# Optimization experiments

Measured on AMD Instinct MI355X. Metric: run time of the kernel, lower is better.

The kernel has to match this reference:

```python
import jax, jax.numpy as jnp
import numpy as np

# --- stochastic-computing constants (match FSUMGUCell defaults) ---
BW_W = 8                      # FSULinearPC weight bitstream bitwidth
BW_M = 4                      # FSUMul bitwidth (shift-register depth)
DEPTH = 10                    # FSUAdd accumulator depth
ACC_MAX = 2.0 ** (DEPTH - 2)  # +256
ACC_MIN = -ACC_MAX
NW = 2 ** BW_W
NM = 2 ** BW_M
# deterministic pseudo-random comparison sequences (stand-in for UnarySim Sobol RNG)
_RNG_W = jnp.asarray(np.random.RandomState(0).permutation(NW), dtype=jnp.float32)
_RNG_WI = jnp.asarray(np.random.RandomState(1).permutation(NW), dtype=jnp.float32)
_RNG_M = jnp.asarray(np.random.RandomState(2).permutation(NM), dtype=jnp.float32)


def _fsu_add(acc, s, offset, scale):
    # FSUAdd (bipolar): accumulate (parallel count - offset), clamp, emit bit when acc >= scale
    acc = jnp.clip(acc + s - offset, ACC_MIN, ACC_MAX)
    out = (acc >= scale).astype(jnp.float32)
    return acc - out * scale, out


def _linear_pc(x_aug, w_src, t):
    # FSULinearPC (bipolar): weight bits generated by rate coding (source > rng[t]),
    # XNOR with input bits, summed into a parallel count. x_aug: [B, F+1] (bias col of 1s).
    wb_p = (w_src > _RNG_W[t % NW]).astype(jnp.float32)   # [O, F+1]
    wb_i = (w_src > _RNG_WI[t % NW]).astype(jnp.float32)
    return x_aug @ wb_p.T + (1.0 - x_aug) @ (1.0 - wb_i).T


def _fsu_mul(state, in0, in1):
    # FSUMul non-static bipolar: estimate P(in1) with a BW_M-bit shift register,
    # regenerate a bit via rng comparison; XNOR-style pos/inv paths gated by in0,
    # with conditionally-advanced rng indices (enable-signal semantics).
    sr, idx_p, idx_i = state
    sr = jnp.concatenate([sr[1:], in1[None]], axis=0)      # shift in newest bit
    cnt = sr.sum(0) * (NM / BW_M)                          # scale count to rng range
    bit_p = (cnt > _RNG_M[idx_p % NM]).astype(jnp.float32)
    bit_i = (cnt > _RNG_M[idx_i % NM]).astype(jnp.float32)
    out = in0 * bit_p + (1.0 - in0) * (1.0 - bit_i)        # disjoint paths -> OR == +
    idx_p = idx_p + in0.astype(jnp.int32)
    idx_i = idx_i + (1 - in0.astype(jnp.int32))
    return (sr, idx_p, idx_i), out


def _w_src(w, b):
    # SourceGen bipolar: binary value in [-1,1] -> integer source in [0, 2^BW_W]
    aug = jnp.concatenate([w, b[:, None]], axis=1)
    return jnp.round((jnp.clip(aug, -1.0, 1.0) + 1.0) * 0.5 * NW)


def _forward(x_bits, hx0, weight_ih, bias_ih, weight_hh, bias_hh):
    T, B, I = x_bits.shape
    H = hx0.shape[1]
    src_ih = _w_src(weight_ih, bias_ih)   # [2H, I+1]
    src_hh = _w_src(weight_hh, bias_hh)   # [2H, H+1]
    ones_col = jnp.ones((B, 1), jnp.float32)
    acc0 = jnp.zeros((B, H), jnp.float32)
    sr0 = jnp.tile((jnp.arange(BW_M) % 2).astype(jnp.float32)[:, None, None], (1, B, H))
    mul0 = (sr0, jnp.zeros((B, H), jnp.int32), jnp.zeros((B, H), jnp.int32))
    off_fg = (I + H + 2 - 1) / 2.0        # entry=I+H+2, scaled=False -> scale=1

    def step(carry, xt):
        h, a1, a2, a3, a4, a5, a6, m1, m2, m3, t = carry
        gate_i = _linear_pc(jnp.concatenate([xt, ones_col], 1), src_ih, t)  # [B, 2H]
        gate_h = _linear_pc(jnp.concatenate([h, ones_col], 1), src_hh, t)
        i_f, i_n = gate_i[:, :H], gate_i[:, H:]
        h_f, h_n = gate_h[:, :H], gate_h[:, H:]
        a1, fg_in = _fsu_add(a1, i_f + h_f, off_fg, 1.0)
        a2, fg = _fsu_add(a2, fg_in + 1.0, 0.0, 2.0)          # scaled (x+1)/2 hardsigmoid
        a3, h_n_bit = _fsu_add(a3, h_n, H / 2.0, 1.0)          # entry=H+1
        m1, ng_prod = _fsu_mul(m1, fg, h_n_bit)
        a4, i_n_bit = _fsu_add(a4, i_n, I / 2.0, 1.0)          # entry=I+1
        a5, ng = _fsu_add(a5, i_n_bit + ng_prod, 0.5, 1.0)     # entry=2
        m2, fgi_prod = _fsu_mul(m2, 1.0 - fg, ng)
        m3, fg_prod = _fsu_mul(m3, fg, h)
        a6, hy = _fsu_add(a6, ng + fgi_prod + fg_prod, 1.0, 1.0)  # entry=3
        return (hy, a1, a2, a3, a4, a5, a6, m1, m2, m3, t + 1), hy

    carry0 = (hx0, acc0, acc0, acc0, acc0, acc0, acc0, mul0, mul0, mul0, jnp.int32(0))
    _, hy_stream = jax.lax.scan(step, carry0, x_bits)
    return hy_stream  # [T, B, H] unary bitstream of hidden state


def setup_inputs():
    key = jax.random.key(0)
    ks = jax.random.split(key, 6)
    T, B, I, H = 64, 128, 1024, 1024
    x_bits = jax.random.bernoulli(ks[0], 0.5, (T, B, I)).astype(jnp.float32)
    hx0 = jax.random.bernoulli(ks[1], 0.5, (B, H)).astype(jnp.float32)
    weight_ih = jax.random.uniform(ks[2], (2 * H, I), jnp.float32, -1.0, 1.0)
    bias_ih = jax.random.uniform(ks[3], (2 * H,), jnp.float32, -1.0, 1.0)
    weight_hh = jax.random.uniform(ks[4], (2 * H, H), jnp.float32, -1.0, 1.0)
    bias_hh = jax.random.uniform(ks[5], (2 * H,), jnp.float32, -1.0, 1.0)
    return {"x_bits": x_bits, "hx0": hx0, "weight_ih": weight_ih, "bias_ih": bias_ih,
            "weight_hh": weight_hh, "bias_hh": bias_hh}


def reference(x_bits, hx0, weight_ih, bias_ih, weight_hh, bias_hh):
    return _forward(x_bits, hx0, weight_ih, bias_ih, weight_hh, bias_hh)
```

## Files before the change

### kernel.cpp

```cpp
#include <hip/hip_runtime.h>


#define NBLK 256
#define NTHR 512

#define WS_BAR_SUB   0u
#define WS_BAR_MST   1024u
#define WS_BAR_FLG   2048u
#define WS_RNGW   8192u
#define WS_RNGWI  9216u
#define WS_RNGM   10240u
#define WS_SRCB   12288u
#define WS_SRCW   20480u
#define WS_XP     8409088u
#define WS_HW     9457664u
#define WS_DT     9523200u
#define WS_MASKS  10571776u

struct SRng {
  unsigned mt[3][624];
  unsigned yb[3][624];
  unsigned draws[3][1248];
  int perm[3][256];
};
struct SC {
  unsigned short rows[16][1028];
  int rngw[64];
  int rngwi[64];
};
struct SL {
  unsigned long long mask2[64*34];
  unsigned xb[32*34];
  unsigned hb[32*34];
  unsigned hraw[64*17];
  int dl[64];
  int rngm[16];
};
union SU { SRng r; SC c; SL l; };

__device__ __forceinline__ unsigned mt_temper(unsigned y){
  y ^= y >> 11;
  y ^= (y << 7)  & 0x9d2c5680u;
  y ^= (y << 15) & 0xefc60000u;
  y ^= y >> 18;
  return y;
}

__device__ void mt_regen_serial(unsigned* mt){
  for (int i = 0; i < 624; i++){
    unsigned y = (mt[i] & 0x80000000u) | (mt[(i+1)%624] & 0x7fffffffu);
    mt[i] = mt[(i+397)%624] ^ (y >> 1) ^ ((y & 1u) ? 0x9908b0dfu : 0u);
  }
}

__device__ void rng_gen(SU* sm, int* rngw, int* rngwi, int* rngm){
  const int tid = threadIdx.x;
  const int wv = tid >> 6, lane = tid & 63;
  const bool act = (wv < 3);
  if (act && lane == 0){
    unsigned* mt = sm->r.mt[wv];
    mt[0] = (unsigned)wv;
    for (int i = 1; i < 624; i++)
      mt[i] = 1812433253u * (mt[i-1] ^ (mt[i-1] >> 30)) + (unsigned)i;
  }
  __syncthreads();
  for (int r = 0; r < 2; r++){
    if (act){
      unsigned* mt = sm->r.mt[wv]; unsigned* yb = sm->r.yb[wv];
      for (int i = lane; i < 623; i += 64)
        yb[i] = (mt[i] & 0x80000000u) | (mt[i+1] & 0x7fffffffu);
    }
    __syncthreads();
    if (act){
      unsigned* mt = sm->r.mt[wv]; unsigned* yb = sm->r.yb[wv];
      for (int i = lane; i < 227; i += 64){
        unsigned y = yb[i];
        mt[i] = mt[i+397] ^ (y >> 1) ^ ((y & 1u) ? 0x9908b0dfu : 0u);
      }
    }
    __syncthreads();
    if (act){
      unsigned* mt = sm->r.mt[wv]; unsigned* yb = sm->r.yb[wv];
      for (int i = 227 + lane; i < 454; i += 64){
        unsigned y = yb[i];
        mt[i] = mt[i-227] ^ (y >> 1) ^ ((y & 1u) ? 0x9908b0dfu : 0u);
      }
    }
    __syncthreads();
    if (act){
      unsigned* mt = sm->r.mt[wv]; unsigned* yb = sm->r.yb[wv];
      for (int i = 454 + lane; i < 624; i += 64){
        unsigned y = (i < 623) ? yb[i]
                   : ((mt[623] & 0x80000000u) | (mt[0] & 0x7fffffffu));
        mt[i] = mt[i-227] ^ (y >> 1) ^ ((y & 1u) ? 0x9908b0dfu : 0u);
      }
    }
    __syncthreads();
    if (act){
      unsigned* mt = sm->r.mt[wv];
      for (int i = lane; i < 624; i += 64)
        sm->r.draws[wv][r*624 + i] = mt_temper(mt[i]);
    }
    __syncthreads();
  }
  if (act && lane == 0){
    const int n = (wv == 2) ? 16 : 256;
    int* perm = sm->r.perm[wv];
    for (int i = 0; i < n; i++) perm[i] = i;
    int dp = 0, spos = 624;
    unsigned* mt = sm->r.mt[wv];
    for (int i = n - 1; i > 0; i--){
      unsigned mask = (unsigned)i;
      mask |= mask >> 1; mask |= mask >> 2; mask |= mask >> 4;
      mask |= mask >> 8; mask |= mask >> 16;
      unsigned v;
      do {
        unsigned d;
        if (dp < 1248) d = sm->r.draws[wv][dp++];
        else {
          if (spos >= 624){ mt_regen_serial(mt); spos = 0; }
          d = mt_temper(mt[spos++]);
        }
        v = d & mask;
      } while (v > (unsigned)i);
      int tmp = perm[i]; perm[i] = perm[v]; perm[v] = tmp;
    }
    int* dst = (wv == 0) ? rngw : (wv == 1) ? rngwi : rngm;
    for (int i = 0; i < n; i++) dst[i] = perm[i];
  }
}

__device__ __forceinline__ void gbar_full(unsigned char* ws, unsigned ep){
  __syncthreads();
  if (threadIdx.x == 0){
    __threadfence();
    unsigned* sub = (unsigned*)(ws + WS_BAR_SUB + (blockIdx.x & 7)*128);
    unsigned old = atomicAdd(sub, 1u);
    if (old == ep*32u - 1u){
      unsigned* mst = (unsigned*)(ws + WS_BAR_MST);
      unsigned mo = atomicAdd(mst, 1u);
      if (mo == ep*8u - 1u){
        for (int i = 0; i < 8; i++)
          __hip_atomic_store((unsigned*)(ws + WS_BAR_FLG + i*128), ep,
                             __ATOMIC_RELAXED, __HIP_MEMORY_SCOPE_AGENT);
      }
    }
    const unsigned* fl = (const unsigned*)(ws + WS_BAR_FLG + (blockIdx.x & 7)*128);
    while (__hip_atomic_load(fl, __ATOMIC_RELAXED, __HIP_MEMORY_SCOPE_AGENT) < ep)
      __builtin_amdgcn_s_sleep(8);
  }
  __syncthreads();
  __threadfence();
}

__device__ __forceinline__ int clampi(int v){
  v = v < -512 ? -512 : v;
  v = v >  512 ?  512 : v;
  return v;
}

__global__ void __launch_bounds__(NTHR)
fsu_kernel(const float* __restrict__ x, const float* __restrict__ hx0,
           const float* __restrict__ wih, const float* __restrict__ bih,
           const float* __restrict__ whh, const float* __restrict__ bhh,
           float* __restrict__ out, unsigned char* __restrict__ ws)
{
  __shared__ SU sm;
  const int tid = threadIdx.x;
  const int bid = blockIdx.x;

  int* rngw  = (int*)(ws + WS_RNGW);
  int* rngwi = (int*)(ws + WS_RNGWI);
  int* rngm  = (int*)(ws + WS_RNGM);
  unsigned short* srcb = (unsigned short*)(ws + WS_SRCB);
  unsigned short* srcw = (unsigned short*)(ws + WS_SRCW);
  unsigned* xp   = (unsigned*)(ws + WS_XP);
  unsigned long long* hw = (unsigned long long*)(ws + WS_HW);
  int* Dt = (int*)(ws + WS_DT);
  unsigned long long* masks = (unsigned long long*)(ws + WS_MASKS);

  if (bid == 0){
    rng_gen(&sm, rngw, rngwi, rngm);
  } else {
    const int gtid = (bid - 1)*NTHR + tid;
    const int lane = tid & 63;
    const int gw = gtid >> 6;
    const int nw = (NBLK-1)*(NTHR/64);
    const int nthr = (NBLK-1)*NTHR;
    for (int ch = gw; ch < 131072; ch += nw){
      float v = x[(size_t)ch*64 + lane];
      unsigned long long bal = __ballot(v != 0.0f);
      if ((lane & 31) == 0) xp[ch*2 + (lane >> 5)] = (unsigned)(bal >> lane);
    }
    for (int idx = gtid; idx < 4096; idx += nthr){
      int bg2 = idx >> 10, jt2 = (idx >> 4) & 63, rp2 = idx & 15;
      int r0 = bg2*32 + 2*rp2;
      unsigned v = 0;
      for (int j = 0; j < 16; j++){
        v |= (hx0[(size_t)r0*1024 + jt2*16 + j] != 0.0f) ? (1u<<j) : 0u;
        v |= (hx0[(size_t)(r0+1)*1024 + jt2*16 + j] != 0.0f) ? (1u<<(16+j)) : 0u;
      }
      hw[idx] = (unsigned long long)v;
    }
    for (int idx = gtid; idx < 4096*1024; idx += nthr){
      int c = idx >> 10, k = idx & 1023;
      float wv2 = (c < 2048) ? wih[(size_t)c*1024 + k] : whh[(size_t)(c - 2048)*1024 + k];
      float cl = fminf(fmaxf(wv2, -1.0f), 1.0f);
      srcw[idx] = (unsigned short)(int)rintf((cl + 1.0f)*0.5f*256.0f);
    }
    for (int c = gtid; c < 4096; c += nthr){
      float bv = (c < 2048) ? bih[c] : bhh[c - 2048];
      float cl = fminf(fmaxf(bv, -1.0f), 1.0f);
      srcb[c] = (unsigned short)(int)rintf((cl + 1.0f)*0.5f*256.0f);
    }
  }
  gbar_full(ws, 1u);

  {
    const int c0 = bid * 16;
    const unsigned* srcw32 = (const unsigned*)srcw;
    for (int q = tid; q < 16*512; q += NTHR){
      int r = q >> 9, w = q & 511;
      ((unsigned*)&sm.c.rows[r][0])[w] = srcw32[(size_t)(c0 + r)*512 + w];
    }
    if (tid < 64) sm.c.rngw[tid] = rngw[tid];
    if (tid >= 64 && tid < 128) sm.c.rngwi[tid - 64] = rngwi[tid - 64];
    __syncthreads();
    for (int rr = 0; rr < 2; rr++){
      int row = tid + rr*NTHR;
      int t = row >> 4, lc = row & 15, col = c0 + lc;
      int rp = sm.c.rngw[t], ri = sm.c.rngwi[t];
      int hi = rp > ri ? rp : ri;
      int lo1 = (rp < ri ? rp : ri) + 1;
      bool rihi = (ri >= rp);
      const unsigned* srow = (const unsigned*)&sm.c.rows[lc][0];
      unsigned long long* gdst = masks + ((size_t)t*4096 + col)*32;
      int cnti = 0;
      for (int w = 0; w < 32; w++){
        unsigned pos = 0, neg = 0;
        #pragma unroll
        for (int i2 = 15; i2 >= 0; i2--){
          unsigned v2 = srow[w*16 + i2];
          int vH = (int)(v2 >> 16);
          int vL = (int)(v2 & 0xFFFFu);
          pos = (pos << 1) | ((unsigned)(hi - vH) >> 31);
          neg = (neg << 1) | ((unsigned)(vH - lo1) >> 31);
          pos = (pos << 1) | ((unsigned)(hi - vL) >> 31);
          neg = (neg << 1) | ((unsigned)(vL - lo1) >> 31);
        }
        gdst[w] = (unsigned long long)pos | ((unsigned long long)neg << 32);
        cnti += rihi ? __popc(pos) : (32 - __popc(neg));
      }
      Dt[t*4096 + col] = 1024 - cnti + (((int)srcb[col] > rp) ? 1 : 0);
    }
  }
  gbar_full(ws, 2u);

  const int jt = bid & 63, bg = bid >> 6;
  const int j0 = jt * 16, b0 = bg * 32;
  const int b_l = tid >> 4, j_l = tid & 15;
  const int bglob = b0 + b_l;

  int hcur = (hx0[(size_t)bglob*1024 + j0 + j_l] != 0.0f) ? 1 : 0;
  int A1=0,A2=0,A3=0,A4=0,A5=0,A6=0;
  unsigned sr1=10u, sr2=10u, sr3=10u;
  int i1p=0,i1i=0,i2p=0,i2i=0,i3p=0,i3i=0;

  if (tid < 16) sm.l.rngm[tid] = rngm[tid];

  const unsigned* msrc = (const unsigned*)masks;
  unsigned* mlds = (unsigned*)sm.l.mask2;

  {
    #pragma unroll
    for (int i = 0; i < 8; i++){
      int q = tid + i*NTHR;
      int r = q >> 6, qq = q & 63;
      int c = (r >> 4)*1024 + j0 + (r & 15);
      mlds[r*68 + qq] = msrc[((size_t)0*4096 + c)*64 + qq];
    }
    #pragma unroll
    for (int i = 0; i < 2; i++){
      int q = tid + i*NTHR;
      int bb = q >> 5, w = q & 31;
      sm.l.xb[bb*34 + w] = xp[((size_t)0*128 + b0 + bb)*32 + w];
    }
    #pragma unroll
    for (int i = 0; i < 2; i++){
      int q = tid + i*NTHR;
      unsigned long long v = __hip_atomic_load(&hw[(size_t)bg*1024 + q],
                                               __ATOMIC_RELAXED,
                                               __HIP_MEMORY_SCOPE_AGENT);
      sm.l.hraw[(q >> 4)*17 + (q & 15)] = (unsigned)v;
    }
    if (tid < 64){
      int c = (tid >> 4)*1024 + j0 + (tid & 15);
      sm.l.dl[tid] = Dt[0*4096 + c];
    }
    __syncthreads();
    #pragma unroll
    for (int i = 0; i < 2; i++){
      int idx = tid + i*NTHR;
      int bb = idx >> 5, w = idx & 31;
      int rp = bb >> 1, sh = (bb & 1) << 4;
      unsigned lo = (sm.l.hraw[(2*w)*17 + rp] >> sh) & 0xFFFFu;
      unsigned hi = (sm.l.hraw[(2*w + 1)*17 + rp] >> sh) & 0xFFFFu;
      sm.l.hb[bb*34 + w] = lo | (hi << 16);
    }
    __syncthreads();
  }

  for (int t = 0; t < 64; t++){
    const int par = t & 1;

    int p0=0,n0=0,p1=0,n1=0,p2=0,n2=0,p3=0,n3=0;
    const ulonglong2* m0p = (const ulonglong2*)&sm.l.mask2[(0*16 + j_l)*34];
    const ulonglong2* m1p = (const ulonglong2*)&sm.l.mask2[(1*16 + j_l)*34];
    const ulonglong2* m2p = (const ulonglong2*)&sm.l.mask2[(2*16 + j_l)*34];
    const ulonglong2* m3p = (const ulonglong2*)&sm.l.mask2[(3*16 + j_l)*34];
    const uint2* xrow = (const uint2*)&sm.l.xb[b_l*34];
    const uint2* hrow = (const uint2*)&sm.l.hb[b_l*34];
    #pragma unroll
    for (int w2 = 0; w2 < 16; w2++){
      uint2 xv = xrow[w2], hv = hrow[w2];
      ulonglong2 a = m0p[w2];
      p0 += __popc(xv.x & (unsigned)a.x) + __popc(xv.y & (unsigned)a.y);
      n0 += __popc(xv.x & (unsigned)(a.x >> 32)) + __popc(xv.y & (unsigned)(a.y >> 32));
      ulonglong2 b = m1p[w2];
      p1 += __popc(xv.x & (unsigned)b.x) + __popc(xv.y & (unsigned)b.y);
      n1 += __popc(xv.x & (unsigned)(b.x >> 32)) + __popc(xv.y & (unsigned)(b.y >> 32));
      ulonglong2 c2 = m2p[w2];
      p2 += __popc(hv.x & (unsigned)c2.x) + __popc(hv.y & (unsigned)c2.y);
      n2 += __popc(hv.x & (unsigned)(c2.x >> 32)) + __popc(hv.y & (unsigned)(c2.y >> 32));
      ulonglong2 d = m3p[w2];
      p3 += __popc(hv.x & (unsigned)d.x) + __popc(hv.y & (unsigned)d.y);
      n3 += __popc(hv.x & (unsigned)(d.x >> 32)) + __popc(hv.y & (unsigned)(d.y >> 32));
    }
    const int g_if = sm.l.dl[0*16 + j_l] + p0 - n0;
    const int g_in = sm.l.dl[1*16 + j_l] + p1 - n1;
    const int g_hf = sm.l.dl[2*16 + j_l] + p2 - n2;
    const int g_hn = sm.l.dl[3*16 + j_l] + p3 - n3;

    int s1 = g_if + g_hf;
    A1 = clampi(A1 + 2*s1 - 2049);
    int fg_in = (A1 >= 2); A1 -= fg_in << 1;
    A2 = clampi(A2 + ((fg_in + 1) << 1));
    int fg = (A2 >= 4); A2 -= fg << 2;
    A3 = clampi(A3 + (g_hn << 1) - 1024);
    int hnb = (A3 >= 2); A3 -= hnb << 1;

    sr1 = ((sr1 >> 1) | ((unsigned)hnb << 3)) & 0xFu;
    int ng_prod;
    {
      int cv = __popc(sr1) << 2;
      int bp = cv > sm.l.rngm[i1p & 15];
      int bi = cv > sm.l.rngm[i1i & 15];
      ng_prod = fg ? bp : (1 - bi);
      i1p += fg; i1i += 1 - fg;
    }
    A4 = clampi(A4 + (g_in << 1) - 1024);
    int inb = (A4 >= 2); A4 -= inb << 1;
    A5 = clampi(A5 + ((inb + ng_prod) << 1) - 1);
    int ng = (A5 >= 2); A5 -= ng << 1;

    sr2 = ((sr2 >> 1) | ((unsigned)ng << 3)) & 0xFu;
    int fgi;
    {
      int cv = __popc(sr2) << 2;
      int bp = cv > sm.l.rngm[i2p & 15];
      int bi = cv > sm.l.rngm[i2i & 15];
      fgi = (1 - fg) ? bp : (1 - bi);
      i2p += 1 - fg; i2i += fg;
    }
    sr3 = ((sr3 >> 1) | ((unsigned)hcur << 3)) & 0xFu;
    int fgp;
    {
      int cv = __popc(sr3) << 2;
      int bp = cv > sm.l.rngm[i3p & 15];
      int bi = cv > sm.l.rngm[i3i & 15];
      fgp = fg ? bp : (1 - bi);
      i3p += fg; i3i += 1 - fg;
    }
    A6 = clampi(A6 + ((ng + fgi + fgp) << 1) - 2);
    int hy = (A6 >= 2); A6 -= hy << 1;
    hcur = hy;

    if (t < 63){
      unsigned long long bal = __ballot(hy);
      if ((tid & 31) == 0){
        unsigned data = (unsigned)(bal >> (tid & 32));
        unsigned long long val = (unsigned long long)data
                               | ((unsigned long long)(unsigned)(t + 1) << 32);
        __hip_atomic_store(
            &hw[(((size_t)(par ^ 1)*4 + bg)*64 + jt)*16 + (tid >> 5)], val,
            __ATOMIC_RELAXED, __HIP_MEMORY_SCOPE_AGENT);
      }
    }
    out[(size_t)t*131072 + (size_t)bglob*1024 + j0 + j_l] = (float)hy;

    if (t < 63){
      __syncthreads();

      unsigned mreg[8], xreg[2];
      int dreg = 0;
      #pragma unroll
      for (int i = 0; i < 8; i++){
        int q = tid + i*NTHR;
        int r = q >> 6, qq = q & 63;
        int c = (r >> 4)*1024 + j0 + (r & 15);
        mreg[i] = msrc[((size_t)(t+1)*4096 + c)*64 + qq];
      }
      #pragma unroll
      for (int i = 0; i < 2; i++){
        int q = tid + i*NTHR;
        int bb = q >> 5, w = q & 31;
        xreg[i] = xp[((size_t)(t+1)*128 + b0 + bb)*32 + w];
      }
      if (tid < 64){
        int c = (tid >> 4)*1024 + j0 + (tid & 15);
        dreg = Dt[(t+1)*4096 + c];
      }

      const unsigned ep = (unsigned)(t + 1);
      if (tid < 64){
        const unsigned long long* slot =
            &hw[(((size_t)(par ^ 1)*4 + bg)*64 + tid)*16];
        while (true){
          unsigned long long v = __hip_atomic_load(slot, __ATOMIC_RELAXED,
                                                   __HIP_MEMORY_SCOPE_AGENT);
          if (__all((int)((unsigned)(v >> 32) >= ep))) break;
          __builtin_amdgcn_s_sleep(2);
        }
      }
      __syncthreads();

      #pragma unroll
      for (int i = 0; i < 2; i++){
        int q = tid + i*NTHR;
        const unsigned long long* slot =
            &hw[((size_t)(par ^ 1)*4 + bg)*1024 + q];
        unsigned long long v;
        while (true){
          v = __hip_atomic_load(slot, __ATOMIC_RELAXED,
                                __HIP_MEMORY_SCOPE_AGENT);
          if ((unsigned)(v >> 32) >= ep) break;
          __builtin_amdgcn_s_sleep(1);
        }
        sm.l.hraw[(q >> 4)*17 + (q & 15)] = (unsigned)v;
      }
      #pragma unroll
      for (int i = 0; i < 8; i++){
        int q = tid + i*NTHR;
        int r = q >> 6, qq = q & 63;
        mlds[r*68 + qq] = mreg[i];
      }
      #pragma unroll
      for (int i = 0; i < 2; i++){
        int q = tid + i*NTHR;
        int bb = q >> 5, w = q & 31;
        sm.l.xb[bb*34 + w] = xreg[i];
      }
      if (tid < 64) sm.l.dl[tid] = dreg;
      __syncthreads();

      #pragma unroll
      for (int i = 0; i < 2; i++){
        int idx = tid + i*NTHR;
        int bb = idx >> 5, w = idx & 31;
        int rp = bb >> 1, sh = (bb & 1) << 4;
        unsigned lo = (sm.l.hraw[(2*w)*17 + rp] >> sh) & 0xFFFFu;
        unsigned hi = (sm.l.hraw[(2*w + 1)*17 + rp] >> sh) & 0xFFFFu;
        sm.l.hb[bb*34 + w] = lo | (hi << 16);
      }
      __syncthreads();
    }
  }
}

extern "C" void kernel_launch(void* const* d_in, const int* in_sizes, int n_in,
                              void* d_out, int out_size, void* d_ws, size_t ws_size,
                              hipStream_t stream)
{
  (void)in_sizes; (void)n_in; (void)out_size; (void)ws_size;
  const float* x   = (const float*)d_in[0];
  const float* hx0 = (const float*)d_in[1];
  const float* wih = (const float*)d_in[2];
  const float* bih = (const float*)d_in[3];
  const float* whh = (const float*)d_in[4];
  const float* bhh = (const float*)d_in[5];
  float* out = (float*)d_out;
  unsigned char* ws = (unsigned char*)d_ws;

  hipMemsetAsync(d_ws, 0, 4096, stream);
  hipMemsetAsync(ws + WS_HW, 0, 65536, stream);

  void* args[] = { (void*)&x, (void*)&hx0, (void*)&wih, (void*)&bih,
                   (void*)&whh, (void*)&bhh, (void*)&out, (void*)&ws };
  hipLaunchCooperativeKernel(reinterpret_cast<void*>(fsu_kernel),
                             dim3(NBLK), dim3(NTHR), args, 0, stream);
}
```

Before: 517.8 us.

## Overlap next-step input popcounts and prefetch with the hidden-state exchange wait

```diff
diff --git a/kernel.cpp b/kernel.cpp
--- a/kernel.cpp
+++ b/kernel.cpp
@@ -29,11 +29,9 @@
   int rngwi[64];
 };
 struct SL {
-  unsigned long long mask2[64*34];
+  unsigned long long mask2[2][64*34];
   unsigned xb[32*34];
-  unsigned hb[32*34];
-  unsigned hraw[64*17];
-  int dl[64];
+  unsigned short hrow16[32*68];
   int rngm[16];
 };
 union SU { SRng r; SC c; SL l; };
@@ -269,15 +267,19 @@
   if (tid < 16) sm.l.rngm[tid] = rngm[tid];
 
   const unsigned* msrc = (const unsigned*)masks;
-  unsigned* mlds = (unsigned*)sm.l.mask2;
+  int cur = 0;
+  int xgf, xgn, dhf, dhn;
+  unsigned mreg[8], xreg[2];
+  int dreg[4];
 
   {
+    unsigned* mbuf = (unsigned*)sm.l.mask2[0];
     #pragma unroll
     for (int i = 0; i < 8; i++){
       int q = tid + i*NTHR;
       int r = q >> 6, qq = q & 63;
       int c = (r >> 4)*1024 + j0 + (r & 15);
-      mlds[r*68 + qq] = msrc[((size_t)0*4096 + c)*64 + qq];
+      mbuf[r*68 + qq] = msrc[((size_t)0*4096 + c)*64 + qq];
     }
     #pragma unroll
     for (int i = 0; i < 2; i++){
@@ -291,57 +293,72 @@
       unsigned long long v = __hip_atomic_load(&hw[(size_t)bg*1024 + q],
                                                __ATOMIC_RELAXED,
                                                __HIP_MEMORY_SCOPE_AGENT);
-      sm.l.hraw[(q >> 4)*17 + (q & 15)] = (unsigned)v;
-    }
-    if (tid < 64){
-      int c = (tid >> 4)*1024 + j0 + (tid & 15);
-      sm.l.dl[tid] = Dt[0*4096 + c];
-    }
-    __syncthreads();
-    #pragma unroll
-    for (int i = 0; i < 2; i++){
-      int idx = tid + i*NTHR;
-      int bb = idx >> 5, w = idx & 31;
-      int rp = bb >> 1, sh = (bb & 1) << 4;
-      unsigned lo = (sm.l.hraw[(2*w)*17 + rp] >> sh) & 0xFFFFu;
-      unsigned hi = (sm.l.hraw[(2*w + 1)*17 + rp] >> sh) & 0xFFFFu;
-      sm.l.hb[bb*34 + w] = lo | (hi << 16);
-    }
-    __syncthreads();
-  }
-
-  for (int t = 0; t < 64; t++){
-    const int par = t & 1;
-
-    int p0=0,n0=0,p1=0,n1=0,p2=0,n2=0,p3=0,n3=0;
-    const ulonglong2* m0p = (const ulonglong2*)&sm.l.mask2[(0*16 + j_l)*34];
-    const ulonglong2* m1p = (const ulonglong2*)&sm.l.mask2[(1*16 + j_l)*34];
-    const ulonglong2* m2p = (const ulonglong2*)&sm.l.mask2[(2*16 + j_l)*34];
-    const ulonglong2* m3p = (const ulonglong2*)&sm.l.mask2[(3*16 + j_l)*34];
+      int jt_ = q >> 4, rp_ = q & 15;
+      unsigned data = (unsigned)v;
+      sm.l.hrow16[(2*rp_)*68 + jt_]   = (unsigned short)(data & 0xFFFFu);
+      sm.l.hrow16[(2*rp_+1)*68 + jt_] = (unsigned short)(data >> 16);
+    }
+    int d0[4];
+    #pragma unroll
+    for (int g = 0; g < 4; g++) d0[g] = Dt[0*4096 + g*1024 + j0 + j_l];
+    __syncthreads();
+    int p0=0,n0=0,p1=0,n1=0;
     const uint2* xrow = (const uint2*)&sm.l.xb[b_l*34];
-    const uint2* hrow = (const uint2*)&sm.l.hb[b_l*34];
+    const ulonglong2* m0p = (const ulonglong2*)&sm.l.mask2[0][(0  + j_l)*34];
+    const ulonglong2* m1p = (const ulonglong2*)&sm.l.mask2[0][(16 + j_l)*34];
     #pragma unroll
     for (int w2 = 0; w2 < 16; w2++){
-      uint2 xv = xrow[w2], hv = hrow[w2];
+      uint2 xv = xrow[w2];
       ulonglong2 a = m0p[w2];
       p0 += __popc(xv.x & (unsigned)a.x) + __popc(xv.y & (unsigned)a.y);
       n0 += __popc(xv.x & (unsigned)(a.x >> 32)) + __popc(xv.y & (unsigned)(a.y >> 32));
       ulonglong2 b = m1p[w2];
       p1 += __popc(xv.x & (unsigned)b.x) + __popc(xv.y & (unsigned)b.y);
       n1 += __popc(xv.x & (unsigned)(b.x >> 32)) + __popc(xv.y & (unsigned)(b.y >> 32));
-      ulonglong2 c2 = m2p[w2];
-      p2 += __popc(hv.x & (unsigned)c2.x) + __popc(hv.y & (unsigned)c2.y);
-      n2 += __popc(hv.x & (unsigned)(c2.x >> 32)) + __popc(hv.y & (unsigned)(c2.y >> 32));
-      ulonglong2 d = m3p[w2];
-      p3 += __popc(hv.x & (unsigned)d.x) + __popc(hv.y & (unsigned)d.y);
-      n3 += __popc(hv.x & (unsigned)(d.x >> 32)) + __popc(hv.y & (unsigned)(d.y >> 32));
-    }
-    const int g_if = sm.l.dl[0*16 + j_l] + p0 - n0;
-    const int g_in = sm.l.dl[1*16 + j_l] + p1 - n1;
-    const int g_hf = sm.l.dl[2*16 + j_l] + p2 - n2;
-    const int g_hn = sm.l.dl[3*16 + j_l] + p3 - n3;
-
-    int s1 = g_if + g_hf;
+    }
+    xgf = d0[0] + p0 - n0;
+    xgn = d0[1] + p1 - n1;
+    dhf = d0[2]; dhn = d0[3];
+    #pragma unroll
+    for (int i = 0; i < 8; i++){
+      int q = tid + i*NTHR;
+      int r = q >> 6, qq = q & 63;
+      int c = (r >> 4)*1024 + j0 + (r & 15);
+      mreg[i] = msrc[((size_t)1*4096 + c)*64 + qq];
+    }
+    #pragma unroll
+    for (int i = 0; i < 2; i++){
+      int q = tid + i*NTHR;
+      int bb = q >> 5, w = q & 31;
+      xreg[i] = xp[((size_t)1*128 + b0 + bb)*32 + w];
+    }
+    #pragma unroll
+    for (int g = 0; g < 4; g++) dreg[g] = Dt[1*4096 + g*1024 + j0 + j_l];
+  }
+
+  for (int t = 0; t < 64; t++){
+    const int par = t & 1;
+
+    int p2=0,n2=0,p3=0,n3=0;
+    {
+      const uint2* hrow = (const uint2*)&sm.l.hrow16[b_l*68];
+      const ulonglong2* m2p = (const ulonglong2*)&sm.l.mask2[cur][(32 + j_l)*34];
+      const ulonglong2* m3p = (const ulonglong2*)&sm.l.mask2[cur][(48 + j_l)*34];
+      #pragma unroll
+      for (int w2 = 0; w2 < 16; w2++){
+        uint2 hv = hrow[w2];
+        ulonglong2 c2 = m2p[w2];
+        p2 += __popc(hv.x & (unsigned)c2.x) + __popc(hv.y & (unsigned)c2.y);
+        n2 += __popc(hv.x & (unsigned)(c2.x >> 32)) + __popc(hv.y & (unsigned)(c2.y >> 32));
+        ulonglong2 d = m3p[w2];
+        p3 += __popc(hv.x & (unsigned)d.x) + __popc(hv.y & (unsigned)d.y);
+        n3 += __popc(hv.x & (unsigned)(d.x >> 32)) + __popc(hv.y & (unsigned)(d.y >> 32));
+      }
+    }
+    const int g_hf = dhf + p2 - n2;
+    const int g_hn = dhn + p3 - n3;
+
+    int s1 = xgf + g_hf;
     A1 = clampi(A1 + 2*s1 - 2049);
     int fg_in = (A1 >= 2); A1 -= fg_in << 1;
     A2 = clampi(A2 + ((fg_in + 1) << 1));
@@ -358,7 +375,7 @@
       ng_prod = fg ? bp : (1 - bi);
       i1p += fg; i1i += 1 - fg;
     }
-    A4 = clampi(A4 + (g_in << 1) - 1024);
+    A4 = clampi(A4 + (xgn << 1) - 1024);
     int inb = (A4 >= 2); A4 -= inb << 1;
     A5 = clampi(A5 + ((inb + ng_prod) << 1) - 1);
     int ng = (A5 >= 2); A5 -= ng << 1;
@@ -392,87 +409,91 @@
         unsigned long long val = (unsigned long long)data
                                | ((unsigned long long)(unsigned)(t + 1) << 32);
         __hip_atomic_store(
-            &hw[(((size_t)(par ^ 1)*4 + bg)*64 + jt)*16 + (tid >> 5)], val,
+            &hw[(((size_t)((par ^ 1)*4 + bg))*64 + jt)*16 + (tid >> 5)], val,
             __ATOMIC_RELAXED, __HIP_MEMORY_SCOPE_AGENT);
       }
     }
     out[(size_t)t*131072 + (size_t)bglob*1024 + j0 + j_l] = (float)hy;
 
     if (t < 63){
+      {
+        unsigned* mbuf = (unsigned*)sm.l.mask2[cur ^ 1];
+        #pragma unroll
+        for (int i = 0; i < 8; i++){
+          int q = tid + i*NTHR;
+          int r = q >> 6, qq = q & 63;
+          mbuf[r*68 + qq] = mreg[i];
+        }
+        #pragma unroll
+        for (int i = 0; i < 2; i++){
+          int q = tid + i*NTHR;
+          int bb = q >> 5, w = q & 31;
+          sm.l.xb[bb*34 + w] = xreg[i];
+        }
+      }
       __syncthreads();
 
-      unsigned mreg[8], xreg[2];
-      int dreg = 0;
-      #pragma unroll
-      for (int i = 0; i < 8; i++){
-        int q = tid + i*NTHR;
-        int r = q >> 6, qq = q & 63;
-        int c = (r >> 4)*1024 + j0 + (r & 15);
-        mreg[i] = msrc[((size_t)(t+1)*4096 + c)*64 + qq];
-      }
-      #pragma unroll
-      for (int i = 0; i < 2; i++){
-        int q = tid + i*NTHR;
-        int bb = q >> 5, w = q & 31;
-        xreg[i] = xp[((size_t)(t+1)*128 + b0 + bb)*32 + w];
-      }
-      if (tid < 64){
-        int c = (tid >> 4)*1024 + j0 + (tid & 15);
-        dreg = Dt[(t+1)*4096 + c];
-      }
-
-      const unsigned ep = (unsigned)(t + 1);
-      if (tid < 64){
-        const unsigned long long* slot =
-            &hw[(((size_t)(par ^ 1)*4 + bg)*64 + tid)*16];
-        while (true){
+      {
+        int p0=0,n0=0,p1=0,n1=0;
+        const uint2* xrow = (const uint2*)&sm.l.xb[b_l*34];
+        const ulonglong2* m0p = (const ulonglong2*)&sm.l.mask2[cur ^ 1][(0  + j_l)*34];
+        const ulonglong2* m1p = (const ulonglong2*)&sm.l.mask2[cur ^ 1][(16 + j_l)*34];
+        #pragma unroll
+        for (int w2 = 0; w2 < 16; w2++){
+          uint2 xv = xrow[w2];
+          ulonglong2 a = m0p[w2];
+          p0 += __popc(xv.x & (unsigned)a.x) + __popc(xv.y & (unsigned)a.y);
+          n0 += __popc(xv.x & (unsigned)(a.x >> 32)) + __popc(xv.y & (unsigned)(a.y >> 32));
+          ulonglong2 b = m1p[w2];
+          p1 += __popc(xv.x & (unsigned)b.x) + __popc(xv.y & (unsigned)b.y);
+          n1 += __popc(xv.x & (unsigned)(b.x >> 32)) + __popc(xv.y & (unsigned)(b.y >> 32));
+        }
+        xgf = dreg[0] + p0 - n0;
+        xgn = dreg[1] + p1 - n1;
+        dhf = dreg[2]; dhn = dreg[3];
+      }
+
+      if (t < 62){
+        #pragma unroll
+        for (int i = 0; i < 8; i++){
+          int q = tid + i*NTHR;
+          int r = q >> 6, qq = q & 63;
+          int c = (r >> 4)*1024 + j0 + (r & 15);
+          mreg[i] = msrc[((size_t)(t+2)*4096 + c)*64 + qq];
+        }
+        #pragma unroll
+        for (int i = 0; i < 2; i++){
+          int q = tid + i*NTHR;
+          int bb = q >> 5, w = q & 31;
+          xreg[i] = xp[((size_t)(t+2)*128 + b0 + bb)*32 + w];
+        }
+        #pragma unroll
+        for (int g = 0; g < 4; g++)
+          dreg[g] = Dt[(t+2)*4096 + g*1024 + j0 + j_l];
+      }
+
+      {
+        const unsigned ep = (unsigned)(t + 1);
+        #pragma unroll
+        for (int i = 0; i < 2; i++){
+          int q = tid + i*NTHR;
+          const unsigned long long* slot =
+              &hw[((size_t)((par ^ 1)*4 + bg))*1024 + q];
           unsigned long long v = __hip_atomic_load(slot, __ATOMIC_RELAXED,
                                                    __HIP_MEMORY_SCOPE_AGENT);
-          if (__all((int)((unsigned)(v >> 32) >= ep))) break;
-          __builtin_amdgcn_s_sleep(2);
+          while ((unsigned)(v >> 32) < ep){
+            __builtin_amdgcn_s_sleep(1);
+            v = __hip_atomic_load(slot, __ATOMIC_RELAXED,
+                                  __HIP_MEMORY_SCOPE_AGENT);
+          }
+          int jt_ = q >> 4, rp_ = q & 15;
+          unsigned data = (unsigned)v;
+          sm.l.hrow16[(2*rp_)*68 + jt_]   = (unsigned short)(data & 0xFFFFu);
+          sm.l.hrow16[(2*rp_+1)*68 + jt_] = (unsigned short)(data >> 16);
         }
       }
       __syncthreads();
-
-      #pragma unroll
-      for (int i = 0; i < 2; i++){
-        int q = tid + i*NTHR;
-        const unsigned long long* slot =
-            &hw[((size_t)(par ^ 1)*4 + bg)*1024 + q];
-        unsigned long long v;
-        while (true){
-          v = __hip_atomic_load(slot, __ATOMIC_RELAXED,
-                                __HIP_MEMORY_SCOPE_AGENT);
-          if ((unsigned)(v >> 32) >= ep) break;
-          __builtin_amdgcn_s_sleep(1);
-        }
-        sm.l.hraw[(q >> 4)*17 + (q & 15)] = (unsigned)v;
-      }
-      #pragma unroll
-      for (int i = 0; i < 8; i++){
-        int q = tid + i*NTHR;
-        int r = q >> 6, qq = q & 63;
-        mlds[r*68 + qq] = mreg[i];
-      }
-      #pragma unroll
-      for (int i = 0; i < 2; i++){
-        int q = tid + i*NTHR;
-        int bb = q >> 5, w = q & 31;
-        sm.l.xb[bb*34 + w] = xreg[i];
-      }
-      if (tid < 64) sm.l.dl[tid] = dreg;
-      __syncthreads();
-
-      #pragma unroll
-      for (int i = 0; i < 2; i++){
-        int idx = tid + i*NTHR;
-        int bb = idx >> 5, w = idx & 31;
-        int rp = bb >> 1, sh = (bb & 1) << 4;
-        unsigned lo = (sm.l.hraw[(2*w)*17 + rp] >> sh) & 0xFFFFu;
-        unsigned hi = (sm.l.hraw[(2*w + 1)*17 + rp] >> sh) & 0xFFFFu;
-        sm.l.hb[bb*34 + w] = lo | (hi << 16);
-      }
-      __syncthreads();
+      cur ^= 1;
     }
   }
 }
```

Result: faster. 497.7 us (-3.9%).
